# Kernel optimization log

Measured on AMD Instinct MI355X. Metric: run time of the kernel, lower is better.

## Reference

```python
import jax, jax.numpy as jnp
import numpy as np

B, T, C, H, DH, L, V = 16, 1023, 384, 6, 64, 6, 256
FF = 4 * C
EPS = 1e-5


def _ln(x, g, b):
    mu = x.mean(-1, keepdims=True)
    var = ((x - mu) ** 2).mean(-1, keepdims=True)
    return (x - mu) * jax.lax.rsqrt(var + EPS) * g + b


def setup_inputs() -> dict:
    key = jax.random.key(0)
    ks = jax.random.split(key, 12)
    n = lambda k, shp: jax.random.normal(k, shp, dtype=jnp.float32) * 0.02
    return {
        "x": jax.random.randint(ks[0], (B, T), 0, V),
        "targets": jax.random.randint(ks[1], (B, T), 0, V),
        "tok_emb": n(ks[2], (V, C)),
        "pos_emb": n(ks[3], (T, C)),
        "Wq": n(ks[4], (L, C, C)), "Wk": n(ks[5], (L, C, C)), "Wv": n(ks[6], (L, C, C)),
        "Wo": n(ks[7], (L, C, C)), "bo": jnp.zeros((L, C)),
        "ln1_g": jnp.ones((L, C)), "ln1_b": jnp.zeros((L, C)),
        "ln2_g": jnp.ones((L, C)), "ln2_b": jnp.zeros((L, C)),
        "W1": n(ks[8], (L, C, FF)), "b1": jnp.zeros((L, FF)),
        "W2": n(ks[9], (L, FF, C)), "b2": jnp.zeros((L, C)),
        "lnf_g": jnp.ones((C,)), "lnf_b": jnp.zeros((C,)),
        "Wf": n(ks[10], (C, V)), "bf": jnp.zeros((V,)),
    }


def _forward(x, targets, tok_emb, pos_emb, Wq, Wk, Wv, Wo, bo,
             ln1_g, ln1_b, ln2_g, ln2_b, W1, b1, W2, b2, lnf_g, lnf_b, Wf, bf):
    h = tok_emb[x] + pos_emb[None, :, :]  # [B,T,C]
    tril = jnp.tril(jnp.ones((T, T), bool))

    def heads(z, W):  # [B,T,C] @ [C,C] -> [B,H,T,DH]
        return jnp.einsum('btc,cd->btd', z, W).reshape(B, T, H, DH).transpose(0, 2, 1, 3)

    def layer(h, p):
        wq, wk, wv, wo, bo_, g1, be1, g2, be2, w1, bb1, w2, bb2 = p
        z = _ln(h, g1, be1)
        q, k, v = heads(z, wq), heads(z, wk), heads(z, wv)
        qk = jnp.einsum('bhtd,bhsd->bhts', q, k) * (DH ** -0.5)
        zm = jnp.where(tril, qk, 0.0)
        # faithful to torch: masked_fill_(zeromask == 0, -inf)
        zm = jnp.where(zm == 0.0, -jnp.inf, zm)
        att = jax.nn.softmax(zm, axis=-1)  # dropout = identity (eval)
        o = jnp.einsum('bhts,bhsd->bhtd', att, v).transpose(0, 2, 1, 3).reshape(B, T, C)
        h = h + jnp.einsum('btc,cd->btd', o, wo) + bo_
        z2 = _ln(h, g2, be2)
        ff = jax.nn.relu(jnp.einsum('btc,cf->btf', z2, w1) + bb1)
        h = h + jnp.einsum('btf,fc->btc', ff, w2) + bb2
        return h, None

    params = (Wq, Wk, Wv, Wo, bo, ln1_g, ln1_b, ln2_g, ln2_b, W1, b1, W2, b2)
    h, _ = jax.lax.scan(layer, h, params)
    logits = jnp.einsum('btc,cv->btv', _ln(h, lnf_g, lnf_b), Wf) + bf
    logits2 = logits.reshape(B * T, V)
    logp = jax.nn.log_softmax(logits2, axis=-1)
    loss = -jnp.take_along_axis(logp, targets.reshape(B * T, 1), axis=1).mean()
    return logits2, loss


def reference(x, targets, tok_emb, pos_emb, Wq, Wk, Wv, Wo, bo,
              ln1_g, ln1_b, ln2_g, ln2_b, W1, b1, W2, b2, lnf_g, lnf_b, Wf, bf):
    return _forward(x, targets, tok_emb, pos_emb, Wq, Wk, Wv, Wo, bo,
                    ln1_g, ln1_b, ln2_g, ln2_b, W1, b1, W2, b2, lnf_g, lnf_b, Wf, bf)
```

## Files before the change

### kernel.cpp

```cpp
#include <hip/hip_runtime.h>
#include <hip/hip_bf16.h>
#include <math.h>

#define B_  16
#define T_  1023
#define C_  384
#define H_  6
#define DH_ 64
#define L_  6
#define V_  256
#define FF_ 1536
#define M_  (B_*T_)
#define MP_ 16384
#define EPS_ 1e-5f

typedef __attribute__((ext_vector_type(8))) short bf16x8;
typedef __attribute__((ext_vector_type(4))) short short4v;
typedef __attribute__((ext_vector_type(4))) float f32x4;

__device__ inline short f2bf(float x) {
    union { float f; unsigned u; } c; c.f = x;
    unsigned r = (c.u + 0x7fffu + ((c.u >> 16) & 1u)) >> 16;
    return (short)r;
}

#define GLDS16(g, l) __builtin_amdgcn_global_load_lds(                         \
    (const __attribute__((address_space(1))) void*)(g),                        \
    (__attribute__((address_space(3))) void*)(l), 16, 0, 0)

#define TRRD(dst, va, IMM) asm volatile("ds_read_b64_tr_b16 %0, %1 offset:" IMM \
    : "=v"(dst) : "v"(va))

__global__ void embed_kernel(const int* __restrict__ x, const float* __restrict__ tok,
                             const float* __restrict__ pos, float* __restrict__ h) {
    int i = blockIdx.x * 256 + threadIdx.x;
    if (i >= M_ * C_) return;
    int bt = i / C_;
    int c  = i - bt * C_;
    int t  = bt % T_;
    h[i] = tok[x[bt] * C_ + c] + pos[t * C_ + c];
}

__global__ __launch_bounds__(256) void wconv_kernel(
    const float* __restrict__ Wq, const float* __restrict__ Wk,
    const float* __restrict__ Wv, const float* __restrict__ Wo,
    const float* __restrict__ W1, const float* __restrict__ W2,
    const float* __restrict__ Wf,
    short* __restrict__ qkvt, short* __restrict__ wot, short* __restrict__ w1t,
    short* __restrict__ w2t, short* __restrict__ wft) {
    __shared__ float tile[32][33];
    int t = blockIdx.x;
    const float* src; short* dst; int K, N, tl;
    if (t < 10368) {
        int l = t / 1728, r = t - l * 1728;
        if (r < 432) {
            int which = r / 144; tl = r - which * 144;
            src = (which == 0 ? Wq : which == 1 ? Wk : Wv) + (size_t)l * 384 * 384;
            dst = qkvt + (size_t)l * 1152 * 384 + (size_t)which * 384 * 384;
            K = 384; N = 384;
        } else if (r < 576) {
            tl = r - 432;
            src = Wo + (size_t)l * 384 * 384; dst = wot + (size_t)l * 384 * 384;
            K = 384; N = 384;
        } else if (r < 1152) {
            tl = r - 576;
            src = W1 + (size_t)l * 384 * 1536; dst = w1t + (size_t)l * 1536 * 384;
            K = 384; N = 1536;
        } else {
            tl = r - 1152;
            src = W2 + (size_t)l * 1536 * 384; dst = w2t + (size_t)l * 384 * 1536;
            K = 1536; N = 384;
        }
    } else {
        tl = t - 10368; src = Wf; dst = wft; K = 384; N = 256;
    }
    int ntx = N >> 5;
    int k0 = (tl / ntx) << 5, n0 = (tl % ntx) << 5;
    int rr = threadIdx.x >> 5, cc = threadIdx.x & 31;
#pragma unroll
    for (int p = 0; p < 4; ++p)
        tile[rr + 8 * p][cc] = src[(size_t)(k0 + rr + 8 * p) * N + n0 + cc];
    __syncthreads();
#pragma unroll
    for (int p = 0; p < 4; ++p)
        dst[(size_t)(n0 + rr + 8 * p) * K + k0 + cc] = f2bf(tile[cc][rr + 8 * p]);
}

__global__ __launch_bounds__(256) void ln_kernel(const float* __restrict__ in,
                                                 const float* __restrict__ g,
                                                 const float* __restrict__ b,
                                                 short* __restrict__ out) {
    int wave = threadIdx.x >> 6, lane = threadIdx.x & 63;
    int row  = blockIdx.x * 4 + wave;
    const float* rp = in + (size_t)row * C_;
    float v[6];
    float s = 0.f, s2 = 0.f;
#pragma unroll
    for (int i = 0; i < 6; ++i) {
        v[i] = rp[i * 64 + lane];
        s  += v[i];
        s2 += v[i] * v[i];
    }
#pragma unroll
    for (int o = 32; o > 0; o >>= 1) {
        s  += __shfl_xor(s,  o, 64);
        s2 += __shfl_xor(s2, o, 64);
    }
    float mu  = s * (1.0f / C_);
    float var = s2 * (1.0f / C_) - mu * mu;
    float rs  = rsqrtf(var + EPS_);
    short* op = out + (size_t)row * C_;
#pragma unroll
    for (int i = 0; i < 6; ++i) {
        int c = i * 64 + lane;
        op[c] = f2bf((v[i] - mu) * rs * g[c] + b[c]);
    }
}

template<int MODE, bool RELU, bool HB>
__global__ __launch_bounds__(256) void mm_kernel(const short* __restrict__ A,
                                                 const short* __restrict__ Bt,
                                                 const float* __restrict__ bias,
                                                 short* __restrict__ outb,
                                                 float* __restrict__ outf,
                                                 int N, int K) {
    __shared__ short Al[2][8][128][8];
    __shared__ short Bl[2][8][128][8];
    int tid  = threadIdx.x;
    int wave = tid >> 6, lane = tid & 63;
    int kg4 = lane >> 4, r16 = lane & 15;
    int wr = (wave >> 1) * 64, wc = (wave & 1) * 64;
    int row0 = blockIdx.x * 128, col0 = blockIdx.y * 128;

    const short* ga = A  + (size_t)(row0 + (tid & 127)) * K + ((tid >> 7) << 5);
    const short* gb = Bt + (size_t)(col0 + (tid & 127)) * K + ((tid >> 7) << 5);
    short* alds = &Al[0][0][0][0];
    short* blds = &Bl[0][0][0][0];
    int ldst = ((tid >> 7) << 2) * 1024 + (tid & 127) * 8;

    f32x4 acc[4][4];
#pragma unroll
    for (int i = 0; i < 4; ++i)
#pragma unroll
        for (int j = 0; j < 4; ++j) { acc[i][j][0]=0.f; acc[i][j][1]=0.f; acc[i][j][2]=0.f; acc[i][j][3]=0.f; }

#define MM_STAGE(BUF)                                                          \
    {                                                                          \
        short* la = alds + (BUF) * 8192 + ldst;                                \
        short* lb = blds + (BUF) * 8192 + ldst;                                \
        GLDS16(ga,      la);        GLDS16(ga + 8,  la + 1024);                \
        GLDS16(ga + 16, la + 2048); GLDS16(ga + 24, la + 3072);                \
        GLDS16(gb,      lb);        GLDS16(gb + 8,  lb + 1024);                \
        GLDS16(gb + 16, lb + 2048); GLDS16(gb + 24, lb + 3072);                \
        ga += 64; gb += 64;                                                    \
    }

#define MM_COMPUTE(BUF)                                                        \
    {                                                                          \
        _Pragma("unroll")                                                      \
        for (int p = 0; p < 2; ++p) {                                          \
            const short* ab = alds + (BUF) * 8192 + (4 * p + kg4) * 1024;      \
            const short* bb = blds + (BUF) * 8192 + (4 * p + kg4) * 1024;      \
            bf16x8 av[4], bv[4];                                               \
            _Pragma("unroll")                                                  \
            for (int i = 0; i < 4; ++i) av[i] = *(const bf16x8*)(ab + (wr + 16*i + r16) * 8); \
            _Pragma("unroll")                                                  \
            for (int j = 0; j < 4; ++j) bv[j] = *(const bf16x8*)(bb + (wc + 16*j + r16) * 8); \
            _Pragma("unroll")                                                  \
            for (int i = 0; i < 4; ++i)                                        \
                _Pragma("unroll")                                              \
                for (int j = 0; j < 4; ++j)                                    \
                    acc[i][j] = __builtin_amdgcn_mfma_f32_16x16x32_bf16(av[i], bv[j], acc[i][j], 0, 0, 0); \
        }                                                                      \
    }

    int NT = K >> 6;
    MM_STAGE(0);
    MM_STAGE(1);
    asm volatile("s_waitcnt vmcnt(8)" ::: "memory");
    __builtin_amdgcn_s_barrier();
    asm volatile("" ::: "memory");

    for (int t = 0; t < NT - 1; ++t) {
        MM_COMPUTE(t & 1);
        __builtin_amdgcn_s_barrier();
        asm volatile("" ::: "memory");
        if (t + 2 < NT) {
            MM_STAGE(t & 1);
            asm volatile("s_waitcnt vmcnt(8)" ::: "memory");
        } else {
            asm volatile("s_waitcnt vmcnt(0)" ::: "memory");
        }
        __builtin_amdgcn_s_barrier();
        asm volatile("" ::: "memory");
    }
    MM_COMPUTE((NT - 1) & 1);
#undef MM_STAGE
#undef MM_COMPUTE

#pragma unroll
    for (int j = 0; j < 4; ++j) {
        int col = col0 + wc + 16 * j + r16;
        float bj = HB ? bias[col] : 0.f;
#pragma unroll
        for (int i = 0; i < 4; ++i) {
#pragma unroll
            for (int rg = 0; rg < 4; ++rg) {
                int row = row0 + wr + 16 * i + 4 * kg4 + rg;
                float v = acc[i][j][rg] + bj;
                if (RELU) v = fmaxf(v, 0.f);
                if (MODE == 0) {
                    outb[(size_t)row * N + col] = f2bf(v);
                } else if (MODE == 1) {
                    outf[(size_t)row * N + col] += v;
                } else {
                    if (row < M_) outf[(size_t)row * N + col] = v;
                }
            }
        }
    }
}

__global__ __launch_bounds__(512) void qkv_kernel(const float* __restrict__ h,
                                                  const float* __restrict__ lng,
                                                  const float* __restrict__ lnb,
                                                  const short* __restrict__ wt,
                                                  short* __restrict__ outb) {
    __shared__ short Zl[48 * 64 * 8];
    int tid  = threadIdx.x;
    int wave = tid >> 6, lane = tid & 63;
    int g = lane >> 4, r16 = lane & 15;
    int r0 = blockIdx.x * 64;

    const short* wbase = wt + (size_t)(16 * wave + r16) * C_ + 8 * g;
    bf16x8 wf[12];
#pragma unroll
    for (int ks = 0; ks < 12; ++ks) wf[ks] = *(const bf16x8*)(wbase + ks * 32);

    float gv6[6], bv6[6];
#pragma unroll
    for (int i = 0; i < 6; ++i) { gv6[i] = lng[i * 64 + lane]; bv6[i] = lnb[i * 64 + lane]; }

    for (int rr = 0; rr < 8; ++rr) {
        int lrow = 8 * wave + rr;
        const float* rp = h + (size_t)(r0 + lrow) * C_;
        float v[6];
        float s = 0.f, s2 = 0.f;
#pragma unroll
        for (int i = 0; i < 6; ++i) {
            v[i] = rp[i * 64 + lane];
            s += v[i]; s2 += v[i] * v[i];
        }
#pragma unroll
        for (int o = 32; o > 0; o >>= 1) {
            s  += __shfl_xor(s,  o, 64);
            s2 += __shfl_xor(s2, o, 64);
        }
        float mu = s * (1.0f / C_);
        float rs = rsqrtf(s2 * (1.0f / C_) - mu * mu + EPS_);
#pragma unroll
        for (int i = 0; i < 6; ++i) {
            int col = i * 64 + lane;
            Zl[(col >> 3) * 512 + lrow * 8 + (col & 7)] =
                f2bf((v[i] - mu) * rs * gv6[i] + bv6[i]);
        }
    }
    __syncthreads();

    for (int c = 0; c < 9; ++c) {
        f32x4 acc[4];
#pragma unroll
        for (int mj = 0; mj < 4; ++mj) { acc[mj][0]=0.f; acc[mj][1]=0.f; acc[mj][2]=0.f; acc[mj][3]=0.f; }
#pragma unroll
        for (int ks = 0; ks < 12; ++ks) {
#pragma unroll
            for (int mj = 0; mj < 4; ++mj) {
                bf16x8 bz = *(const bf16x8*)(Zl + ((4 * ks + g) * 64 + 16 * mj + r16) * 8);
                acc[mj] = __builtin_amdgcn_mfma_f32_16x16x32_bf16(wf[ks], bz, acc[mj], 0, 0, 0);
            }
        }
        if (c + 1 < 9) {
#pragma unroll
            for (int ks = 0; ks < 12; ++ks)
                wf[ks] = *(const bf16x8*)(wbase + (size_t)(c + 1) * 128 * C_ + ks * 32);
        }
#pragma unroll
        for (int mj = 0; mj < 4; ++mj) {
            short4v ov;
#pragma unroll
            for (int rg = 0; rg < 4; ++rg) ov[rg] = f2bf(acc[mj][rg]);
            *(short4v*)(outb + (size_t)(r0 + 16 * mj + r16) * 1152
                        + 128 * c + 16 * wave + 4 * g) = ov;
        }
    }
}

__global__ __launch_bounds__(512) void wo_kernel(const short* __restrict__ ob,
                                                 const short* __restrict__ wt,
                                                 const float* __restrict__ bo,
                                                 float* __restrict__ h,
                                                 const float* __restrict__ lng,
                                                 const float* __restrict__ lnb,
                                                 short* __restrict__ zout) {
    __shared__ short Ol[48 * 64 * 8];
    int tid  = threadIdx.x;
    int wave = tid >> 6, lane = tid & 63;
    int g = lane >> 4, r16 = lane & 15;
    int r0 = blockIdx.x * 64;

    {
        const short* go = ob + (size_t)(r0 + lane) * C_ + wave * 8;
        short* lo = Ol + (wave * 64 + lane) * 8;
#pragma unroll
        for (int ro = 0; ro < 6; ++ro) { GLDS16(go, lo); go += 64; lo += 4096; }
    }

    const short* wbase = wt + (size_t)(48 * wave + r16) * C_ + 8 * g;
    bf16x8 wf[12];
#pragma unroll
    for (int ks2 = 0; ks2 < 4; ++ks2)
#pragma unroll
        for (int j = 0; j < 3; ++j)
            wf[ks2 * 3 + j] = *(const bf16x8*)(wbase + (size_t)(16 * j) * C_ + 32 * ks2);

    asm volatile("s_waitcnt vmcnt(0)" ::: "memory");
    __builtin_amdgcn_s_barrier();
    asm volatile("" ::: "memory");

    f32x4 acc[4][3];
#pragma unroll
    for (int mi = 0; mi < 4; ++mi)
#pragma unroll
        for (int j = 0; j < 3; ++j) { acc[mi][j][0]=0.f; acc[mi][j][1]=0.f; acc[mi][j][2]=0.f; acc[mi][j][3]=0.f; }

    for (int kc = 0; kc < 3; ++kc) {
#pragma unroll
        for (int ks2 = 0; ks2 < 4; ++ks2) {
            bf16x8 pa[4];
#pragma unroll
            for (int mi = 0; mi < 4; ++mi)
                pa[mi] = *(const bf16x8*)(Ol + ((16 * kc + 4 * ks2 + g) * 64 + 16 * mi + r16) * 8);
#pragma unroll
            for (int j = 0; j < 3; ++j)
#pragma unroll
                for (int mi = 0; mi < 4; ++mi)
                    acc[mi][j] = __builtin_amdgcn_mfma_f32_16x16x32_bf16(pa[mi], wf[ks2 * 3 + j], acc[mi][j], 0, 0, 0);
        }
        if (kc + 1 < 3) {
#pragma unroll
            for (int ks2 = 0; ks2 < 4; ++ks2)
#pragma unroll
                for (int j = 0; j < 3; ++j)
                    wf[ks2 * 3 + j] = *(const bf16x8*)(wbase + (size_t)(16 * j) * C_
                                                       + 128 * (kc + 1) + 32 * ks2);
        }
    }
    __syncthreads();

    float rsum[4][4], rsq[4][4];
#pragma unroll
    for (int mi = 0; mi < 4; ++mi)
#pragma unroll
        for (int rg = 0; rg < 4; ++rg) { rsum[mi][rg] = 0.f; rsq[mi][rg] = 0.f; }

#pragma unroll
    for (int j = 0; j < 3; ++j) {
        int col = 48 * wave + 16 * j + r16;
        float bj = bo[col];
#pragma unroll
        for (int mi = 0; mi < 4; ++mi) {
#pragma unroll
            for (int rg = 0; rg < 4; ++rg) {
                int row = r0 + 16 * mi + 4 * g + rg;
                float hv = h[(size_t)row * C_ + col] + acc[mi][j][rg] + bj;
                h[(size_t)row * C_ + col] = hv;
                acc[mi][j][rg] = hv;
                rsum[mi][rg] += hv;
                rsq[mi][rg]  += hv * hv;
            }
        }
    }
#pragma unroll
    for (int o = 1; o < 16; o <<= 1) {
#pragma unroll
        for (int mi = 0; mi < 4; ++mi)
#pragma unroll
            for (int rg = 0; rg < 4; ++rg) {
                rsum[mi][rg] += __shfl_xor(rsum[mi][rg], o, 64);
                rsq[mi][rg]  += __shfl_xor(rsq[mi][rg],  o, 64);
            }
    }
    float* St = (float*)Ol;
    if (r16 == 0) {
#pragma unroll
        for (int mi = 0; mi < 4; ++mi)
#pragma unroll
            for (int rg = 0; rg < 4; ++rg) {
                int rr = 16 * mi + 4 * g + rg;
                St[rr * 16 + 2 * wave]     = rsum[mi][rg];
                St[rr * 16 + 2 * wave + 1] = rsq[mi][rg];
            }
    }
    __syncthreads();
    if (tid < 64) {
        float s = 0.f, s2 = 0.f;
#pragma unroll
        for (int w = 0; w < 8; ++w) { s += St[tid * 16 + 2 * w]; s2 += St[tid * 16 + 2 * w + 1]; }
        float mu  = s * (1.0f / C_);
        float var = s2 * (1.0f / C_) - mu * mu;
        St[tid * 16]     = mu;
        St[tid * 16 + 1] = rsqrtf(var + EPS_);
    }
    __syncthreads();
#pragma unroll
    for (int j = 0; j < 3; ++j) {
        int col = 48 * wave + 16 * j + r16;
        float gam = lng[col], bet = lnb[col];
#pragma unroll
        for (int mi = 0; mi < 4; ++mi) {
#pragma unroll
            for (int rg = 0; rg < 4; ++rg) {
                int rr = 16 * mi + 4 * g + rg;
                float mu = St[rr * 16], rs = St[rr * 16 + 1];
                zout[(size_t)(r0 + rr) * C_ + col] = f2bf((acc[mi][j][rg] - mu) * rs * gam + bet);
            }
        }
    }
}

__global__ __launch_bounds__(512) void ffn_kernel(const short* __restrict__ z,
                                                  const short* __restrict__ w1t,
                                                  const short* __restrict__ w2t,
                                                  const float* __restrict__ b1,
                                                  const float* __restrict__ b2,
                                                  float* __restrict__ h) {
    __shared__ short Zl[48 * 64 * 8];
    __shared__ short Pl[16 * 64 * 8];
    int tid  = threadIdx.x;
    int wave = tid >> 6, lane = tid & 63;
    int g = lane >> 4, r16 = lane & 15;
    int r0 = blockIdx.x * 64;

    {
        const short* gz = z + (size_t)(r0 + lane) * C_ + wave * 8;
        short* lz = Zl + (wave * 64 + lane) * 8;
#pragma unroll
        for (int ro = 0; ro < 6; ++ro) {
            GLDS16(gz, lz);
            gz += 64;
            lz += 8 * 64 * 8;
        }
    }

    const short* w1base = w1t + (size_t)(16 * wave + r16) * C_ + 8 * g;
    const short* w2base = w2t + (size_t)(48 * wave + r16) * FF_ + 8 * g;

    bf16x8 w1f[12];
#pragma unroll
    for (int ks = 0; ks < 12; ++ks)
        w1f[ks] = *(const bf16x8*)(w1base + ks * 32);

    asm volatile("s_waitcnt vmcnt(0)" ::: "memory");
    __builtin_amdgcn_s_barrier();
    asm volatile("" ::: "memory");

    f32x4 acc2[4][3];
#pragma unroll
    for (int mi = 0; mi < 4; ++mi)
#pragma unroll
        for (int j = 0; j < 3; ++j) { acc2[mi][j][0]=0.f; acc2[mi][j][1]=0.f; acc2[mi][j][2]=0.f; acc2[mi][j][3]=0.f; }

    for (int c = 0; c < 12; ++c) {
        bf16x8 w2f[12];
#pragma unroll
        for (int ks2 = 0; ks2 < 4; ++ks2)
#pragma unroll
            for (int j = 0; j < 3; ++j)
                w2f[ks2 * 3 + j] = *(const bf16x8*)(w2base + (size_t)(16 * j) * FF_
                                                    + 128 * c + 32 * ks2);

        f32x4 acc1[4];
#pragma unroll
        for (int mj = 0; mj < 4; ++mj) { acc1[mj][0]=0.f; acc1[mj][1]=0.f; acc1[mj][2]=0.f; acc1[mj][3]=0.f; }
#pragma unroll
        for (int ks = 0; ks < 12; ++ks) {
#pragma unroll
            for (int mj = 0; mj < 4; ++mj) {
                bf16x8 bz = *(const bf16x8*)(Zl + ((4 * ks + g) * 64 + 16 * mj + r16) * 8);
                acc1[mj] = __builtin_amdgcn_mfma_f32_16x16x32_bf16(w1f[ks], bz, acc1[mj], 0, 0, 0);
            }
        }
        f32x4 b1v = *(const f32x4*)(b1 + 128 * c + 16 * wave + 4 * g);
        int oct = 2 * wave + (g >> 1);
#pragma unroll
        for (int mj = 0; mj < 4; ++mj) {
            short4v pv;
#pragma unroll
            for (int rg = 0; rg < 4; ++rg)
                pv[rg] = f2bf(fmaxf(acc1[mj][rg] + b1v[rg], 0.f));
            *(short4v*)(Pl + (oct * 64 + 16 * mj + r16) * 8 + (g & 1) * 4) = pv;
        }
        __syncthreads();

        if (c + 1 < 12) {
#pragma unroll
            for (int ks = 0; ks < 12; ++ks)
                w1f[ks] = *(const bf16x8*)(w1base + (size_t)(c + 1) * 128 * C_ + ks * 32);
        }

#pragma unroll
        for (int ks2 = 0; ks2 < 4; ++ks2) {
            bf16x8 pa[4];
#pragma unroll
            for (int mi = 0; mi < 4; ++mi)
                pa[mi] = *(const bf16x8*)(Pl + ((4 * ks2 + g) * 64 + 16 * mi + r16) * 8);
#pragma unroll
            for (int j = 0; j < 3; ++j) {
#pragma unroll
                for (int mi = 0; mi < 4; ++mi)
                    acc2[mi][j] = __builtin_amdgcn_mfma_f32_16x16x32_bf16(pa[mi], w2f[ks2 * 3 + j], acc2[mi][j], 0, 0, 0);
            }
        }
        __syncthreads();
    }

#pragma unroll
    for (int j = 0; j < 3; ++j) {
        int col = 48 * wave + 16 * j + r16;
        float bj = b2[col];
#pragma unroll
        for (int mi = 0; mi < 4; ++mi) {
#pragma unroll
            for (int rg = 0; rg < 4; ++rg) {
                int row = r0 + 16 * mi + 4 * g + rg;
                h[(size_t)row * C_ + col] += acc2[mi][j][rg] + bj;
            }
        }
    }
}

__device__ __forceinline__ void attn_step(int kt, int qg, int g, int r16,
                                          const char* Kb, unsigned ka, unsigned va,
                                          short (*Pw)[40],
                                          bf16x8 qf0, bf16x8 qf1,
                                          f32x4* o_acc, float& m, float& l) {
    f32x4 s0, s1;
    s0[0]=0.f;s0[1]=0.f;s0[2]=0.f;s0[3]=0.f;
    s1[0]=0.f;s1[1]=0.f;s1[2]=0.f;s1[3]=0.f;
    bf16x8 a00 = *(const bf16x8*)(Kb + ka);
    bf16x8 a01 = *(const bf16x8*)(Kb + (ka ^ 64u));
    bf16x8 a10 = *(const bf16x8*)(Kb + ka + 2048u);
    bf16x8 a11 = *(const bf16x8*)(Kb + ((ka + 2048u) ^ 64u));
    s0 = __builtin_amdgcn_mfma_f32_16x16x32_bf16(a00, qf0, s0, 0, 0, 0);
    s0 = __builtin_amdgcn_mfma_f32_16x16x32_bf16(a01, qf1, s0, 0, 0, 0);
    s1 = __builtin_amdgcn_mfma_f32_16x16x32_bf16(a10, qf0, s1, 0, 0, 0);
    s1 = __builtin_amdgcn_mfma_f32_16x16x32_bf16(a11, qf1, s1, 0, 0, 0);

    int kb0 = kt * 32 + 4 * g;
    float sv[8];
#pragma unroll
    for (int r = 0; r < 4; ++r) {
        sv[r]     = (kb0 + r      <= qg) ? s0[r] * 0.125f : -3e38f;
        sv[4 + r] = (kb0 + 16 + r <= qg) ? s1[r] * 0.125f : -3e38f;
    }
    float pmax = sv[0];
#pragma unroll
    for (int i = 1; i < 8; ++i) pmax = fmaxf(pmax, sv[i]);
    pmax = fmaxf(pmax, __shfl_xor(pmax, 16, 64));
    pmax = fmaxf(pmax, __shfl_xor(pmax, 32, 64));
    float mn   = fmaxf(m, pmax);
    float corr = __expf(m - mn);
    float rs = 0.f;
    short pb[8];
#pragma unroll
    for (int i = 0; i < 8; ++i) {
        float p = __expf(sv[i] - mn);
        rs += p;
        pb[i] = f2bf(p);
    }
    rs += __shfl_xor(rs, 16, 64);
    rs += __shfl_xor(rs, 32, 64);
    l = l * corr + rs;
    m = mn;

    short4v t0w, t1w;
    t0w[0]=pb[0]; t0w[1]=pb[1]; t0w[2]=pb[2]; t0w[3]=pb[3];
    t1w[0]=pb[4]; t1w[1]=pb[5]; t1w[2]=pb[6]; t1w[3]=pb[7];
    *(short4v*)&Pw[r16][4 * g]      = t0w;
    *(short4v*)&Pw[r16][16 + 4 * g] = t1w;

    short4v v0, v1, v2, v3, v4, v5, v6, v7;
    TRRD(v0, va, "0");    TRRD(v1, va, "512");
    TRRD(v2, va, "128");  TRRD(v3, va, "640");
    TRRD(v4, va, "256");  TRRD(v5, va, "768");
    TRRD(v6, va, "384");  TRRD(v7, va, "896");

    bf16x8 pB = *(const bf16x8*)&Pw[r16][8 * g];
#pragma unroll
    for (int d = 0; d < 4; ++d) {
        o_acc[d][0] *= corr; o_acc[d][1] *= corr;
        o_acc[d][2] *= corr; o_acc[d][3] *= corr;
    }
    asm volatile("s_waitcnt lgkmcnt(0)" ::: "memory");
    __builtin_amdgcn_sched_barrier(0);

    bf16x8 av0, av1, av2, av3;
#pragma unroll
    for (int i = 0; i < 4; ++i) {
        av0[i] = v0[i]; av0[i + 4] = v1[i];
        av1[i] = v2[i]; av1[i + 4] = v3[i];
        av2[i] = v4[i]; av2[i + 4] = v5[i];
        av3[i] = v6[i]; av3[i + 4] = v7[i];
    }
    o_acc[0] = __builtin_amdgcn_mfma_f32_16x16x32_bf16(av0, pB, o_acc[0], 0, 0, 0);
    o_acc[1] = __builtin_amdgcn_mfma_f32_16x16x32_bf16(av1, pB, o_acc[1], 0, 0, 0);
    o_acc[2] = __builtin_amdgcn_mfma_f32_16x16x32_bf16(av2, pB, o_acc[2], 0, 0, 0);
    o_acc[3] = __builtin_amdgcn_mfma_f32_16x16x32_bf16(av3, pB, o_acc[3], 0, 0, 0);
}

__global__ __launch_bounds__(256) void attn_kernel(const short* __restrict__ qkv,
                                                   short* __restrict__ o) {
    __shared__ short Kl[2][32 * 64];
    __shared__ short Vl[2][32 * 64];
    __shared__ short P_lds[4][16][40];

    int tid  = threadIdx.x;
    int wave = tid >> 6;
    int lane = tid & 63;
    int g    = lane >> 4;
    int r16  = lane & 15;

    int qtA = blockIdx.x;
    int qtB = 15 - qtA;
    int bh = blockIdx.y;
    int b  = bh / H_, hh = bh - b * H_;
    size_t rbase = (size_t)b * T_;
    int qoff = hh * 64;

    int q0A = qtA * 64, q0B = qtB * 64;
    int qgA = q0A + wave * 16 + r16;
    int qgB = q0B + wave * 16 + r16;

    const short* qrA = qkv + (rbase + qgA) * 1152 + qoff;
    const short* qrB = qkv + (rbase + qgB) * 1152 + qoff;
    bf16x8 qfA0 = *(const bf16x8*)(qrA + 8 * g);
    bf16x8 qfA1 = *(const bf16x8*)(qrA + 32 + 8 * g);
    bf16x8 qfB0 = *(const bf16x8*)(qrB + 8 * g);
    bf16x8 qfB1 = *(const bf16x8*)(qrB + 32 + 8 * g);

    int kkey = tid >> 3;
    int koct = (tid & 7) ^ (kkey & 7);
    const short* gk = qkv + (rbase + kkey) * 1152 + qoff + 384 + koct * 8;
    int vkey = 4 * (tid >> 5) + ((tid >> 1) & 3);
    int voct = 2 * ((tid >> 3) & 3) + (tid & 1);
    const short* gv = qkv + (rbase + vkey) * 1152 + qoff + 768 + voct * 8;
    short* lk0 = Kl[0] + tid * 8;
    short* lk1 = Kl[1] + tid * 8;
    short* lv0 = Vl[0] + tid * 8;
    short* lv1 = Vl[1] + tid * 8;

    f32x4 oA[4], oB[4];
#pragma unroll
    for (int d = 0; d < 4; ++d) {
        oA[d][0]=0.f; oA[d][1]=0.f; oA[d][2]=0.f; oA[d][3]=0.f;
        oB[d][0]=0.f; oB[d][1]=0.f; oB[d][2]=0.f; oB[d][3]=0.f;
    }
    float mA = -3e38f, lA = 0.f, mB = -3e38f, lB = 0.f;

    const char* Kb0 = (const char*)Kl[0];
    const char* Kb1 = (const char*)Kl[1];
    unsigned ka = (unsigned)(r16 * 128 + ((g ^ (r16 & 7)) << 4));
    unsigned va0 = (unsigned)(size_t)(__attribute__((address_space(3))) short*)Vl[0]
                 + 1024u * (unsigned)g + 8u * (unsigned)r16;
    unsigned va1 = va0 + 4096u;

    int ktA_hi = (q0A + wave * 16 + 15) >> 5;
    int ktB_hi = (q0B + wave * 16 + 15) >> 5;
    int nkt = 2 * (qtB + 1);

    GLDS16(gk, lk0);
    GLDS16(gv, lv0);
    gk += 32 * 1152; gv += 32 * 1152;
    asm volatile("s_waitcnt vmcnt(0)" ::: "memory");
    __builtin_amdgcn_s_barrier();
    asm volatile("" ::: "memory");

    for (int kt = 0; kt < nkt; ++kt) {
        int cur = kt & 1;
        if (kt + 1 < nkt) {
            GLDS16(gk, cur ? lk0 : lk1);
            GLDS16(gv, cur ? lv0 : lv1);
            gk += 32 * 1152; gv += 32 * 1152;
        }
        const char* Kb = cur ? Kb1 : Kb0;
        unsigned va = cur ? va1 : va0;

        if (kt <= ktB_hi)
            attn_step(kt, qgB, g, r16, Kb, ka, va, P_lds[wave], qfB0, qfB1, oB, mB, lB);
        if (kt <= ktA_hi)
            attn_step(kt, qgA, g, r16, Kb, ka, va, P_lds[wave], qfA0, qfA1, oA, mA, lA);

        asm volatile("s_waitcnt vmcnt(0)" ::: "memory");
        __builtin_amdgcn_s_barrier();
        asm volatile("" ::: "memory");
    }

    {
        float inv = (lA > 0.f) ? 1.f / lA : 0.f;
        short* orow = o + (rbase + qgA) * C_ + qoff;
#pragma unroll
        for (int d = 0; d < 4; ++d) {
            short4v ov;
#pragma unroll
            for (int r = 0; r < 4; ++r) ov[r] = f2bf(oA[d][r] * inv);
            *(short4v*)(orow + 16 * d + 4 * g) = ov;
        }
    }
    if (qgB < T_) {
        float inv = (lB > 0.f) ? 1.f / lB : 0.f;
        short* orow = o + (rbase + qgB) * C_ + qoff;
#pragma unroll
        for (int d = 0; d < 4; ++d) {
            short4v ov;
#pragma unroll
            for (int r = 0; r < 4; ++r) ov[r] = f2bf(oB[d][r] * inv);
            *(short4v*)(orow + 16 * d + 4 * g) = ov;
        }
    }
}

__global__ __launch_bounds__(256) void nll_kernel(const float* __restrict__ logits,
                                                  const int* __restrict__ tgt,
                                                  float* __restrict__ nll) {
    int wave = threadIdx.x >> 6, lane = threadIdx.x & 63;
    int row  = blockIdx.x * 4 + wave;
    const float* rp = logits + (size_t)row * V_;
    float v[4];
    float mx = -INFINITY;
#pragma unroll
    for (int i = 0; i < 4; ++i) {
        v[i] = rp[i * 64 + lane];
        mx = fmaxf(mx, v[i]);
    }
#pragma unroll
    for (int o = 32; o > 0; o >>= 1) mx = fmaxf(mx, __shfl_xor(mx, o, 64));
    float s = 0.f;
#pragma unroll
    for (int i = 0; i < 4; ++i) s += expf(v[i] - mx);
#pragma unroll
    for (int o = 32; o > 0; o >>= 1) s += __shfl_xor(s, o, 64);
    if (lane == 0) {
        float lse = mx + logf(s);
        nll[row] = lse - rp[tgt[row]];
    }
}

__global__ __launch_bounds__(256) void loss_kernel(const float* __restrict__ nll,
                                                   float* __restrict__ loss) {
    __shared__ float sm[256];
    float s = 0.f;
    for (int i = threadIdx.x; i < M_; i += 256) s += nll[i];
    sm[threadIdx.x] = s;
    __syncthreads();
    for (int o = 128; o > 0; o >>= 1) {
        if (threadIdx.x < o) sm[threadIdx.x] += sm[threadIdx.x + o];
        __syncthreads();
    }
    if (threadIdx.x == 0) *loss = sm[0] * (1.0f / M_);
}

extern "C" void kernel_launch(void* const* d_in, const int* in_sizes, int n_in,
                              void* d_out, int out_size, void* d_ws, size_t ws_size,
                              hipStream_t stream) {
    const int*   x       = (const int*)d_in[0];
    const int*   targets = (const int*)d_in[1];
    const float* tok_emb = (const float*)d_in[2];
    const float* pos_emb = (const float*)d_in[3];
    const float* Wq      = (const float*)d_in[4];
    const float* Wk      = (const float*)d_in[5];
    const float* Wv      = (const float*)d_in[6];
    const float* Wo      = (const float*)d_in[7];
    const float* bo      = (const float*)d_in[8];
    const float* ln1_g   = (const float*)d_in[9];
    const float* ln1_b   = (const float*)d_in[10];
    const float* ln2_g   = (const float*)d_in[11];
    const float* ln2_b   = (const float*)d_in[12];
    const float* W1      = (const float*)d_in[13];
    const float* b1      = (const float*)d_in[14];
    const float* W2      = (const float*)d_in[15];
    const float* b2      = (const float*)d_in[16];
    const float* lnf_g   = (const float*)d_in[17];
    const float* lnf_b   = (const float*)d_in[18];
    const float* Wf      = (const float*)d_in[19];
    const float* bf      = (const float*)d_in[20];

    float* logits = (float*)d_out;
    float* loss   = logits + (size_t)M_ * V_;

    float* h    = (float*)d_ws;
    short* z    = (short*)(h + (size_t)MP_ * C_);
    short* big  = z + (size_t)MP_ * C_;
    short* ob   = big + (size_t)MP_ * FF_;
    short* qkvt = ob + (size_t)MP_ * C_;
    short* wot  = qkvt + (size_t)L_ * 1152 * 384;
    short* w1t  = wot + (size_t)L_ * 384 * 384;
    short* w2t  = w1t + (size_t)L_ * 1536 * 384;
    short* wft  = w2t + (size_t)L_ * 1536 * 384;
    float* nll  = (float*)(wft + (size_t)256 * 384);

    wconv_kernel<<<10464, 256, 0, stream>>>(Wq, Wk, Wv, Wo, W1, W2, Wf,
                                            qkvt, wot, w1t, w2t, wft);
    embed_kernel<<<(M_ * C_ + 255) / 256, 256, 0, stream>>>(x, tok_emb, pos_emb, h);

    for (int l = 0; l < L_; ++l) {
        qkv_kernel<<<MP_ / 64, 512, 0, stream>>>(
            h, ln1_g + l * C_, ln1_b + l * C_,
            qkvt + (size_t)l * 1152 * 384, big);
        attn_kernel<<<dim3(8, B_ * H_), 256, 0, stream>>>(big, ob);
        wo_kernel<<<MP_ / 64, 512, 0, stream>>>(
            ob, wot + (size_t)l * 384 * 384, bo + l * C_, h,
            ln2_g + l * C_, ln2_b + l * C_, z);
        ffn_kernel<<<MP_ / 64, 512, 0, stream>>>(
            z, w1t + (size_t)l * 1536 * 384, w2t + (size_t)l * 384 * 1536,
            b1 + l * FF_, b2 + l * C_, h);
    }

    ln_kernel<<<M_ / 4, 256, 0, stream>>>(h, lnf_g, lnf_b, z);
    mm_kernel<2, false, true><<<dim3(128, 2), 256, 0, stream>>>(
        z, wft, bf, nullptr, logits, 256, 384);

    nll_kernel<<<M_ / 4, 256, 0, stream>>>(logits, targets, nll);
    loss_kernel<<<1, 256, 0, stream>>>(nll, loss);
}
```

Baseline: 1.225 ms.

## Fuse final layernorm, vocab projection and NLL into one kernel

Replaces the separate final LN, logits GEMM and NLL kernels with a single kernel. Each block normalizes 64 rows into LDS, multiplies them by register-held Wf fragments with MFMA, writes logits, and computes log-softmax NLL from an LDS copy of the logits. This removes the bf16 z round trip, the re-read of logits and two launches, at the cost of more LDS per block and possibly lower occupancy.

```diff
diff --git a/kernel.cpp b/kernel.cpp
--- a/kernel.cpp
+++ b/kernel.cpp
@@ -86,141 +86,6 @@
         dst[(size_t)(n0 + rr + 8 * p) * K + k0 + cc] = f2bf(tile[cc][rr + 8 * p]);
 }
 
-__global__ __launch_bounds__(256) void ln_kernel(const float* __restrict__ in,
-                                                 const float* __restrict__ g,
-                                                 const float* __restrict__ b,
-                                                 short* __restrict__ out) {
-    int wave = threadIdx.x >> 6, lane = threadIdx.x & 63;
-    int row  = blockIdx.x * 4 + wave;
-    const float* rp = in + (size_t)row * C_;
-    float v[6];
-    float s = 0.f, s2 = 0.f;
-#pragma unroll
-    for (int i = 0; i < 6; ++i) {
-        v[i] = rp[i * 64 + lane];
-        s  += v[i];
-        s2 += v[i] * v[i];
-    }
-#pragma unroll
-    for (int o = 32; o > 0; o >>= 1) {
-        s  += __shfl_xor(s,  o, 64);
-        s2 += __shfl_xor(s2, o, 64);
-    }
-    float mu  = s * (1.0f / C_);
-    float var = s2 * (1.0f / C_) - mu * mu;
-    float rs  = rsqrtf(var + EPS_);
-    short* op = out + (size_t)row * C_;
-#pragma unroll
-    for (int i = 0; i < 6; ++i) {
-        int c = i * 64 + lane;
-        op[c] = f2bf((v[i] - mu) * rs * g[c] + b[c]);
-    }
-}
-
-template<int MODE, bool RELU, bool HB>
-__global__ __launch_bounds__(256) void mm_kernel(const short* __restrict__ A,
-                                                 const short* __restrict__ Bt,
-                                                 const float* __restrict__ bias,
-                                                 short* __restrict__ outb,
-                                                 float* __restrict__ outf,
-                                                 int N, int K) {
-    __shared__ short Al[2][8][128][8];
-    __shared__ short Bl[2][8][128][8];
-    int tid  = threadIdx.x;
-    int wave = tid >> 6, lane = tid & 63;
-    int kg4 = lane >> 4, r16 = lane & 15;
-    int wr = (wave >> 1) * 64, wc = (wave & 1) * 64;
-    int row0 = blockIdx.x * 128, col0 = blockIdx.y * 128;
-
-    const short* ga = A  + (size_t)(row0 + (tid & 127)) * K + ((tid >> 7) << 5);
-    const short* gb = Bt + (size_t)(col0 + (tid & 127)) * K + ((tid >> 7) << 5);
-    short* alds = &Al[0][0][0][0];
-    short* blds = &Bl[0][0][0][0];
-    int ldst = ((tid >> 7) << 2) * 1024 + (tid & 127) * 8;
-
-    f32x4 acc[4][4];
-#pragma unroll
-    for (int i = 0; i < 4; ++i)
-#pragma unroll
-        for (int j = 0; j < 4; ++j) { acc[i][j][0]=0.f; acc[i][j][1]=0.f; acc[i][j][2]=0.f; acc[i][j][3]=0.f; }
-
-#define MM_STAGE(BUF)                                                          \
-    {                                                                          \
-        short* la = alds + (BUF) * 8192 + ldst;                                \
-        short* lb = blds + (BUF) * 8192 + ldst;                                \
-        GLDS16(ga,      la);        GLDS16(ga + 8,  la + 1024);                \
-        GLDS16(ga + 16, la + 2048); GLDS16(ga + 24, la + 3072);                \
-        GLDS16(gb,      lb);        GLDS16(gb + 8,  lb + 1024);                \
-        GLDS16(gb + 16, lb + 2048); GLDS16(gb + 24, lb + 3072);                \
-        ga += 64; gb += 64;                                                    \
-    }
-
-#define MM_COMPUTE(BUF)                                                        \
-    {                                                                          \
-        _Pragma("unroll")                                                      \
-        for (int p = 0; p < 2; ++p) {                                          \
-            const short* ab = alds + (BUF) * 8192 + (4 * p + kg4) * 1024;      \
-            const short* bb = blds + (BUF) * 8192 + (4 * p + kg4) * 1024;      \
-            bf16x8 av[4], bv[4];                                               \
-            _Pragma("unroll")                                                  \
-            for (int i = 0; i < 4; ++i) av[i] = *(const bf16x8*)(ab + (wr + 16*i + r16) * 8); \
-            _Pragma("unroll")                                                  \
-            for (int j = 0; j < 4; ++j) bv[j] = *(const bf16x8*)(bb + (wc + 16*j + r16) * 8); \
-            _Pragma("unroll")                                                  \
-            for (int i = 0; i < 4; ++i)                                        \
-                _Pragma("unroll")                                              \
-                for (int j = 0; j < 4; ++j)                                    \
-                    acc[i][j] = __builtin_amdgcn_mfma_f32_16x16x32_bf16(av[i], bv[j], acc[i][j], 0, 0, 0); \
-        }                                                                      \
-    }
-
-    int NT = K >> 6;
-    MM_STAGE(0);
-    MM_STAGE(1);
-    asm volatile("s_waitcnt vmcnt(8)" ::: "memory");
-    __builtin_amdgcn_s_barrier();
-    asm volatile("" ::: "memory");
-
-    for (int t = 0; t < NT - 1; ++t) {
-        MM_COMPUTE(t & 1);
-        __builtin_amdgcn_s_barrier();
-        asm volatile("" ::: "memory");
-        if (t + 2 < NT) {
-            MM_STAGE(t & 1);
-            asm volatile("s_waitcnt vmcnt(8)" ::: "memory");
-        } else {
-            asm volatile("s_waitcnt vmcnt(0)" ::: "memory");
-        }
-        __builtin_amdgcn_s_barrier();
-        asm volatile("" ::: "memory");
-    }
-    MM_COMPUTE((NT - 1) & 1);
-#undef MM_STAGE
-#undef MM_COMPUTE
-
-#pragma unroll
-    for (int j = 0; j < 4; ++j) {
-        int col = col0 + wc + 16 * j + r16;
-        float bj = HB ? bias[col] : 0.f;
-#pragma unroll
-        for (int i = 0; i < 4; ++i) {
-#pragma unroll
-            for (int rg = 0; rg < 4; ++rg) {
-                int row = row0 + wr + 16 * i + 4 * kg4 + rg;
-                float v = acc[i][j][rg] + bj;
-                if (RELU) v = fmaxf(v, 0.f);
-                if (MODE == 0) {
-                    outb[(size_t)row * N + col] = f2bf(v);
-                } else if (MODE == 1) {
-                    outf[(size_t)row * N + col] += v;
-                } else {
-                    if (row < M_) outf[(size_t)row * N + col] = v;
-                }
-            }
-        }
-    }
-}
-
 __global__ __launch_bounds__(512) void qkv_kernel(const float* __restrict__ h,
                                                   const float* __restrict__ lng,
                                                   const float* __restrict__ lnb,
@@ -535,6 +400,114 @@
                 int row = r0 + 16 * mi + 4 * g + rg;
                 h[(size_t)row * C_ + col] += acc2[mi][j][rg] + bj;
             }
+        }
+    }
+}
+
+__global__ __launch_bounds__(512) void final_kernel(const float* __restrict__ h,
+                                                    const float* __restrict__ lng,
+                                                    const float* __restrict__ lnb,
+                                                    const short* __restrict__ wt,
+                                                    const float* __restrict__ bf,
+                                                    const int* __restrict__ tgt,
+                                                    float* __restrict__ logits,
+                                                    float* __restrict__ nll) {
+    __shared__ short Zl[48 * 64 * 8];
+    __shared__ float Lg[64][260];
+    int tid  = threadIdx.x;
+    int wave = tid >> 6, lane = tid & 63;
+    int g = lane >> 4, r16 = lane & 15;
+    int r0 = blockIdx.x * 64;
+
+    const short* wbase = wt + (size_t)(16 * wave + r16) * C_ + 8 * g;
+    bf16x8 wf[12];
+#pragma unroll
+    for (int ks = 0; ks < 12; ++ks) wf[ks] = *(const bf16x8*)(wbase + ks * 32);
+
+    float gv6[6], bv6[6];
+#pragma unroll
+    for (int i = 0; i < 6; ++i) { gv6[i] = lng[i * 64 + lane]; bv6[i] = lnb[i * 64 + lane]; }
+
+    for (int rr = 0; rr < 8; ++rr) {
+        int lrow = 8 * wave + rr;
+        const float* rp = h + (size_t)(r0 + lrow) * C_;
+        float v[6];
+        float s = 0.f, s2 = 0.f;
+#pragma unroll
+        for (int i = 0; i < 6; ++i) {
+            v[i] = rp[i * 64 + lane];
+            s += v[i]; s2 += v[i] * v[i];
+        }
+#pragma unroll
+        for (int o = 32; o > 0; o >>= 1) {
+            s  += __shfl_xor(s,  o, 64);
+            s2 += __shfl_xor(s2, o, 64);
+        }
+        float mu = s * (1.0f / C_);
+        float rs = rsqrtf(s2 * (1.0f / C_) - mu * mu + EPS_);
+#pragma unroll
+        for (int i = 0; i < 6; ++i) {
+            int col = i * 64 + lane;
+            Zl[(col >> 3) * 512 + lrow * 8 + (col & 7)] =
+                f2bf((v[i] - mu) * rs * gv6[i] + bv6[i]);
+        }
+    }
+    __syncthreads();
+
+    for (int c = 0; c < 2; ++c) {
+        f32x4 acc[4];
+#pragma unroll
+        for (int mj = 0; mj < 4; ++mj) { acc[mj][0]=0.f; acc[mj][1]=0.f; acc[mj][2]=0.f; acc[mj][3]=0.f; }
+#pragma unroll
+        for (int ks = 0; ks < 12; ++ks) {
+#pragma unroll
+            for (int mj = 0; mj < 4; ++mj) {
+                bf16x8 bz = *(const bf16x8*)(Zl + ((4 * ks + g) * 64 + 16 * mj + r16) * 8);
+                acc[mj] = __builtin_amdgcn_mfma_f32_16x16x32_bf16(wf[ks], bz, acc[mj], 0, 0, 0);
+            }
+        }
+        if (c + 1 < 2) {
+#pragma unroll
+            for (int ks = 0; ks < 12; ++ks)
+                wf[ks] = *(const bf16x8*)(wbase + (size_t)128 * C_ + ks * 32);
+        }
+        int colb = 128 * c + 16 * wave + 4 * g;
+        f32x4 bv4 = *(const f32x4*)(bf + colb);
+#pragma unroll
+        for (int mj = 0; mj < 4; ++mj) {
+            int lrow = 16 * mj + r16;
+            int row  = r0 + lrow;
+            f32x4 ov;
+#pragma unroll
+            for (int rg = 0; rg < 4; ++rg) {
+                ov[rg] = acc[mj][rg] + bv4[rg];
+                Lg[lrow][colb + rg] = ov[rg];
+            }
+            if (row < M_) *(f32x4*)(logits + (size_t)row * V_ + colb) = ov;
+        }
+    }
+    __syncthreads();
+
+    for (int rr = 0; rr < 8; ++rr) {
+        int lrow = 8 * wave + rr;
+        int row  = r0 + lrow;
+        float v[4];
+        float mx = -INFINITY;
+#pragma unroll
+        for (int i = 0; i < 4; ++i) {
+            v[i] = Lg[lrow][i * 64 + lane];
+            mx = fmaxf(mx, v[i]);
+        }
+#pragma unroll
+        for (int o = 32; o > 0; o >>= 1) mx = fmaxf(mx, __shfl_xor(mx, o, 64));
+        float s = 0.f;
+#pragma unroll
+        for (int i = 0; i < 4; ++i) s += expf(v[i] - mx);
+#pragma unroll
+        for (int o = 32; o > 0; o >>= 1) s += __shfl_xor(s, o, 64);
+        if (lane == 0 && row < M_) {
+            float lse = mx + logf(s);
+            nll[row] = lse - Lg[lrow][tgt[row]];
         }
     }
 }
@@ -726,32 +699,6 @@
             for (int r = 0; r < 4; ++r) ov[r] = f2bf(oB[d][r] * inv);
             *(short4v*)(orow + 16 * d + 4 * g) = ov;
         }
-    }
-}
-
-__global__ __launch_bounds__(256) void nll_kernel(const float* __restrict__ logits,
-                                                  const int* __restrict__ tgt,
-                                                  float* __restrict__ nll) {
-    int wave = threadIdx.x >> 6, lane = threadIdx.x & 63;
-    int row  = blockIdx.x * 4 + wave;
-    const float* rp = logits + (size_t)row * V_;
-    float v[4];
-    float mx = -INFINITY;
-#pragma unroll
-    for (int i = 0; i < 4; ++i) {
-        v[i] = rp[i * 64 + lane];
-        mx = fmaxf(mx, v[i]);
-    }
-#pragma unroll
-    for (int o = 32; o > 0; o >>= 1) mx = fmaxf(mx, __shfl_xor(mx, o, 64));
-    float s = 0.f;
-#pragma unroll
-    for (int i = 0; i < 4; ++i) s += expf(v[i] - mx);
-#pragma unroll
-    for (int o = 32; o > 0; o >>= 1) s += __shfl_xor(s, o, 64);
-    if (lane == 0) {
-        float lse = mx + logf(s);
-        nll[row] = lse - rp[tgt[row]];
     }
 }
 
@@ -825,10 +772,7 @@
             b1 + l * FF_, b2 + l * C_, h);
     }
 
-    ln_kernel<<<M_ / 4, 256, 0, stream>>>(h, lnf_g, lnf_b, z);
-    mm_kernel<2, false, true><<<dim3(128, 2), 256, 0, stream>>>(
-        z, wft, bf, nullptr, logits, 256, 384);
-
-    nll_kernel<<<M_ / 4, 256, 0, stream>>>(logits, targets, nll);
+    final_kernel<<<MP_ / 64, 512, 0, stream>>>(
+        h, lnf_g, lnf_b, wft, bf, targets, logits, nll);
     loss_kernel<<<1, 256, 0, stream>>>(nll, loss);
 }
```

Result: no change. 1.211 ms (-1.1%).
